# Kernel tuning notes

Measured on AMD Instinct MI355X. Metric: run time of the kernel, lower is better.

## Reference

```python
import jax, jax.numpy as jnp
import numpy as np

D_MODEL = 128
K_RED = 3          # fd_redundancy_k
MAX_ITERS = 16     # upper bound on the data-dependent while-loop; masked no-ops after convergence
NEG = -1e9


def setup_inputs() -> dict:
    key = jax.random.key(0)
    ks = jax.random.split(key, 10)
    B, U, S, D, F = 16, 2048, 512, D_MODEL, 32
    return {
        "user_enc": jax.random.normal(ks[0], (B, U, D), jnp.float32),
        "server_enc": jax.random.normal(ks[1], (B, S, D), jnp.float32),
        "users": jax.random.uniform(ks[2], (B, U, 6), jnp.float32),
        "servers": jax.random.uniform(ks[3], (B, S, 7), jnp.float32),
        "connect": jax.random.randint(ks[4], (B, U, S), 0, 2, jnp.int32),
        "fd_onehot": jax.random.randint(ks[5], (B, S, F), 0, 2, jnp.int32),
        "state_proj_w": jax.random.normal(ks[6], (D, 4), jnp.float32) * 0.05,
        "state_proj_b": jnp.zeros((D,), jnp.float32),
        "fd_bias": jnp.asarray(1.0, jnp.float32),
        "ptr_q_w": jax.random.normal(ks[7], (D, D), jnp.float32) * (D ** -0.5),
        "ptr_k_w": jax.random.normal(ks[8], (D, D), jnp.float32) * (D ** -0.5),
        "user_state_w": jax.random.normal(ks[9], (1, 3), jnp.float32) * 0.05,
        "score_bias": jnp.zeros((1,), jnp.float32),
    }


def _forward(user_enc, server_enc, users, servers, connect, fd_onehot,
             state_proj_w, state_proj_b, fd_bias, ptr_q_w, ptr_k_w,
             user_state_w, score_bias):
    B, U, _ = users.shape
    S = servers.shape[1]
    D = user_enc.shape[-1]
    needs = users[..., 2:6]                    # [B,U,4]
    init_cap = servers[..., 3:7]               # [B,S,4]
    connect_mask = connect.astype(bool)
    fd = fd_onehot.astype(jnp.float32)         # [B,S,F] in {0,1}
    F = fd.shape[-1]
    inv_sqrt_d = D ** -0.5
    tk = jnp.float32(max(K_RED, 1))
    q = user_enc @ ptr_q_w.T                   # [B,U,D]  (loop-invariant)
    u_ids = jnp.arange(U)
    s_ids = jnp.arange(S)

    def body(carry, _):
        alloc, cap, seen, logp, flag = carry
        replica_count = alloc.sum(-1)                                    # [B,U]
        need_more = replica_count < K_RED
        can_fulfill = jnp.all(cap[:, None] >= needs[:, :, None], axis=-1)  # [B,U,S]
        eligible = connect_mask & can_fulfill & need_more[..., None] & ~alloc
        go = flag & jnp.any(need_more) & jnp.any(eligible)

        # pointer-attention logits with dynamic server state
        is_new_fd = (jnp.einsum('buf,bsf->bus', seen, fd) < 0.5).astype(jnp.float32)
        cap_ratio = cap / jnp.maximum(init_cap, 1e-6)
        k_vec = (server_enc + cap_ratio @ state_proj_w.T + state_proj_b) @ ptr_k_w.T
        logits = jnp.einsum('bud,bsd->bus', q, k_vec) * inv_sqrt_d + score_bias
        logits = logits + fd_bias * is_new_fd
        rc = replica_count.astype(jnp.float32)
        user_state = jnp.stack([rc / tk,
                                jnp.clip(K_RED - rc, 0.0, None) / tk,
                                (replica_count == K_RED - 1).astype(jnp.float32)], axis=-1)
        logits = logits + user_state @ user_state_w.T                    # broadcast [B,U,1]

        cand = jnp.where(eligible, logits, NEG)
        # each valid server greedily proposes its best eligible user
        valid_server = jnp.any(eligible, axis=1)                         # [B,S]
        prop_u = jnp.argmax(cand, axis=1)                                # [B,S]
        prop_mask = valid_server[:, None, :] & (u_ids[None, :, None] == prop_u[:, None, :])
        logp_prop = jnp.max(cand, axis=1) - jax.nn.logsumexp(cand, axis=1)  # [B,S]

        # each proposed user accepts the highest-scoring proposing server
        acc_cand = jnp.where(prop_mask, logits, NEG)
        has_prop = jnp.any(prop_mask, axis=2)                            # [B,U]
        chosen_s = jnp.argmax(acc_cand, axis=2)                          # [B,U]
        accepted = has_prop[..., None] & (s_ids == chosen_s[..., None])  # [B,U,S]

        alloc = alloc | (accepted & go)
        fd_gain = (jnp.einsum('bus,bsf->buf', prop_mask.astype(jnp.float32), fd) > 0).astype(jnp.float32)
        seen = jnp.where(go, jnp.maximum(seen, fd_gain), seen)
        used = jnp.einsum('bus,buc->bsc', accepted.astype(jnp.float32), needs)
        cap = jnp.where(go, jnp.maximum(cap - used, 0.0), cap)
        gathered = jnp.take_along_axis(logp_prop, chosen_s, axis=1)      # [B,U]
        logp = logp + jnp.where(go & has_prop, gathered, 0.0)
        return (alloc, cap, seen, logp, go), None

    init = (jnp.zeros((B, U, S), bool), init_cap,
            jnp.zeros((B, U, F), jnp.float32), jnp.zeros((B, U), jnp.float32),
            jnp.asarray(True))
    (alloc, cap, seen, logp, _), _ = jax.lax.scan(body, init, None, length=MAX_ITERS)
    return logp.sum(axis=1), alloc, cap


def reference(user_enc, server_enc, users, servers, connect, fd_onehot,
              state_proj_w, state_proj_b, fd_bias, ptr_q_w, ptr_k_w,
              user_state_w, score_bias):
    # policy='greedy' branch of the original forward
    return _forward(user_enc, server_enc, users, servers, connect, fd_onehot,
                    state_proj_w, state_proj_b, fd_bias, ptr_q_w, ptr_k_w,
                    user_state_w, score_bias)
```

## Files before the change

### kernel.cpp

```cpp
#include <hip/hip_runtime.h>
#include <hip/hip_bf16.h>

#define B_N 16
#define U_N 2048
#define S_N 512
#define D_N 128
#define INV_SQRT_D 0.08838834764831845f

typedef unsigned long long ull;
typedef __attribute__((ext_vector_type(8))) short bf16x8;
typedef __attribute__((ext_vector_type(4))) float f32x4;
typedef __attribute__((ext_vector_type(4))) _Float16 f16x4;

__device__ __forceinline__ unsigned monof(float v) {
    unsigned b = __float_as_uint(v);
    return (b & 0x80000000u) ? ~b : (b | 0x80000000u);
}
__device__ __forceinline__ float unmonof(unsigned m) {
    unsigned b = (m & 0x80000000u) ? (m & 0x7fffffffu) : ~m;
    return __uint_as_float(b);
}
__device__ __forceinline__ unsigned short f2bf(float x) {
    unsigned u = __float_as_uint(x);
    return (unsigned short)((u + 0x7fffu + ((u >> 16) & 1u)) >> 16);
}

__global__ void init_state(const float* __restrict__ servers, const float* __restrict__ users,
                           const int* __restrict__ fd_onehot,
                           uint4* alloc3, unsigned* rcArr, unsigned* seenArr,
                           float* logp, float* capA, float* invA, unsigned* fdm, float* nds,
                           unsigned* frozen, float* out) {
    int i = blockIdx.x * 256 + threadIdx.x;
    if (i < B_N * U_N) {
        rcArr[i] = 0u; seenArr[i] = 0u; logp[i] = 0.f;
        alloc3[i] = make_uint4(0xFFFFFFFFu, 0xFFFFFFFFu, 0xFFFFFFFFu, 0xFFFFFFFFu);
        const float* up = users + (size_t)i * 6;
        nds[i * 4 + 0] = up[2]; nds[i * 4 + 1] = up[3];
        nds[i * 4 + 2] = up[4]; nds[i * 4 + 3] = up[5];
    }
    if (i < B_N * S_N) {
        const float* sp = servers + (size_t)i * 7;
        float4 c = make_float4(sp[3], sp[4], sp[5], sp[6]);
        ((float4*)capA)[i] = c;
        ((float4*)invA)[i] = make_float4(1.f / fmaxf(c.x, 1e-6f), 1.f / fmaxf(c.y, 1e-6f),
                                         1.f / fmaxf(c.z, 1e-6f), 1.f / fmaxf(c.w, 1e-6f));
        unsigned w = 0u;
        const int* fp = fd_onehot + (size_t)i * 32;
        #pragma unroll
        for (int f = 0; f < 32; ++f) w |= (fp[f] != 0 ? 1u : 0u) << f;
        fdm[i] = w;
    }
    if (i < 16) { frozen[i] = 0u; out[i] = 0.f; }
}

__global__ void pack_connect(const int* __restrict__ connect, ull* __restrict__ connU) {
    int i = blockIdx.x * 4 + (threadIdx.x >> 6);
    int lane = threadIdx.x & 63;
    const int* row = connect + (size_t)i * S_N;
    #pragma unroll
    for (int c = 0; c < 8; ++c) {
        ull m = __ballot(row[c * 64 + lane] != 0);
        if (lane == 0) connU[(size_t)i * 8 + c] = m;
    }
}

template <bool ABIAS, int OUTMODE>
__global__ __launch_bounds__(256) void gemm_nt(const float* __restrict__ A, const float* __restrict__ Bm,
                                               const float* __restrict__ abias, float* __restrict__ C,
                                               unsigned short* __restrict__ C16,
                                               int M, int N, int K, float scale) {
    __shared__ float As[16][68];
    __shared__ float Bs[16][68];
    int z = blockIdx.z;
    const float* Ab = A + (size_t)z * M * K;
    const float* Bb = Bm;
    int m0 = blockIdx.x * 64, n0 = blockIdx.y * 64;
    int tid = threadIdx.x;
    int tx = tid & 15, ty = tid >> 4;
    int lrow = tid >> 2, lk = (tid & 3) * 4;
    float acc[4][4] = {};
    for (int k0 = 0; k0 < K; k0 += 16) {
        float4 av = *(const float4*)(Ab + (size_t)(m0 + lrow) * K + k0 + lk);
        float4 bv = *(const float4*)(Bb + (size_t)(n0 + lrow) * K + k0 + lk);
        if (ABIAS) {
            av.x += abias[k0 + lk]; av.y += abias[k0 + lk + 1];
            av.z += abias[k0 + lk + 2]; av.w += abias[k0 + lk + 3];
        }
        __syncthreads();
        As[lk + 0][lrow] = av.x; As[lk + 1][lrow] = av.y; As[lk + 2][lrow] = av.z; As[lk + 3][lrow] = av.w;
        Bs[lk + 0][lrow] = bv.x; Bs[lk + 1][lrow] = bv.y; Bs[lk + 2][lrow] = bv.z; Bs[lk + 3][lrow] = bv.w;
        __syncthreads();
        #pragma unroll
        for (int kk = 0; kk < 16; ++kk) {
            float4 a = *(const float4*)&As[kk][ty * 4];
            float4 bq = *(const float4*)&Bs[kk][tx * 4];
            float ar[4] = {a.x, a.y, a.z, a.w}, br[4] = {bq.x, bq.y, bq.z, bq.w};
            #pragma unroll
            for (int ii = 0; ii < 4; ++ii)
                #pragma unroll
                for (int jj = 0; jj < 4; ++jj) acc[ii][jj] += ar[ii] * br[jj];
        }
    }
    #pragma unroll
    for (int ii = 0; ii < 4; ++ii) {
        float4 o = make_float4(acc[ii][0] * scale, acc[ii][1] * scale,
                               acc[ii][2] * scale, acc[ii][3] * scale);
        size_t idx = (size_t)z * M * N + (size_t)(m0 + ty * 4 + ii) * N + n0 + tx * 4;
        if (OUTMODE != 1) *(float4*)(C + idx) = o;
        if (OUTMODE != 0) {
            ushort4 ob;
            ob.x = f2bf(o.x); ob.y = f2bf(o.y); ob.z = f2bf(o.z); ob.w = f2bf(o.w);
            *(ushort4*)(C16 + idx) = ob;
        }
    }
}

__global__ void m3_kernel(const float* __restrict__ kw, const float* __restrict__ spw,
                          const float* __restrict__ qw, float* __restrict__ M3) {
    __shared__ float M2s[512];
    int t = threadIdx.x;
    {
        int d = t >> 2, c = t & 3;
        float acc = 0.f;
        for (int e = 0; e < 128; ++e) acc += kw[d * 128 + e] * spw[e * 4 + c];
        M2s[d * 4 + c] = acc * INV_SQRT_D;
    }
    __syncthreads();
    {
        int e = t >> 2, c = t & 3;
        float acc = 0.f;
        for (int d = 0; d < 128; ++d) acc += qw[d * 128 + e] * M2s[d * 4 + c];
        M3[e * 4 + c] = acc;
    }
}

__global__ void qm_kernel(const float* __restrict__ enc, const float* __restrict__ M3, float* __restrict__ qm) {
    __shared__ float qs[64][129];
    __shared__ float m3s[512];
    int b = blockIdx.y, u0 = blockIdx.x * 64;
    int t = threadIdx.x;
    for (int i = t; i < 512; i += 256) m3s[i] = M3[i];
    #pragma unroll
    for (int it = 0; it < 8; ++it) {
        int f4 = t + 256 * it;
        int row = f4 >> 5;
        int col = (f4 & 31) * 4;
        float4 v = *(const float4*)(enc + ((size_t)(b * U_N + u0 + row)) * D_N + col);
        qs[row][col] = v.x; qs[row][col + 1] = v.y; qs[row][col + 2] = v.z; qs[row][col + 3] = v.w;
    }
    __syncthreads();
    int ul = t >> 2, c = t & 3;
    float acc = 0.f;
    for (int d = 0; d < 128; ++d) acc += qs[ul][d] * m3s[d * 4 + c];
    qm[((size_t)(b * U_N + u0 + ul)) * 4 + c] = acc;
}

__global__ __launch_bounds__(256) void qk_mfma(const unsigned short* __restrict__ qb,
                                               const unsigned short* __restrict__ kb,
                                               _Float16* __restrict__ qkh) {
    const int b = blockIdx.z, u0 = blockIdx.x * 128, s0 = blockIdx.y * 64;
    const int t = threadIdx.x, w = t >> 6, l = t & 63;
    const int lr = l & 15, lq = l >> 4;
    const unsigned short* Ab = qb + ((size_t)(b * U_N + u0 + w * 32 + lr)) * D_N + lq * 8;
    const unsigned short* Bb = kb + ((size_t)(b * S_N + s0 + lr)) * D_N + lq * 8;
    f32x4 acc[2][4] = {};
    #pragma unroll
    for (int kt = 0; kt < 4; ++kt) {
        bf16x8 a0 = *(const bf16x8*)(Ab + kt * 32);
        bf16x8 a1 = *(const bf16x8*)(Ab + 16 * D_N + kt * 32);
        #pragma unroll
        for (int c = 0; c < 4; ++c) {
            bf16x8 bf = *(const bf16x8*)(Bb + c * 16 * D_N + kt * 32);
            acc[0][c] = __builtin_amdgcn_mfma_f32_16x16x32_bf16(a0, bf, acc[0][c], 0, 0, 0);
            acc[1][c] = __builtin_amdgcn_mfma_f32_16x16x32_bf16(a1, bf, acc[1][c], 0, 0, 0);
        }
    }
    __shared__ _Float16 Cs[128][72];
    #pragma unroll
    for (int mt = 0; mt < 2; ++mt)
        #pragma unroll
        for (int c = 0; c < 4; ++c)
            #pragma unroll
            for (int r = 0; r < 4; ++r)
                Cs[w * 32 + mt * 16 + lq * 4 + r][c * 16 + lr] = (_Float16)acc[mt][c][r];
    __syncthreads();
    #pragma unroll
    for (int k = 0; k < 4; ++k) {
        int row = (t >> 3) + k * 32;
        int sg = (t & 7) * 8;
        uint4 v = *(const uint4*)&Cs[row][sg];
        *(uint4*)(qkh + ((size_t)(b * U_N + u0 + row)) * S_N + s0 + sg) = v;
    }
}

__global__ __launch_bounds__(1024) void iter_fused(
    const _Float16* __restrict__ qkh, const float* __restrict__ qm4,
    const float* __restrict__ nds, const unsigned* __restrict__ connU32,
    const unsigned* __restrict__ fdm_, float* __restrict__ capA,
    const float* __restrict__ invA, const float* __restrict__ usw,
    const float* __restrict__ sbp, const float* __restrict__ fdbp,
    uint4* __restrict__ alloc3, unsigned* __restrict__ rcArr,
    unsigned* __restrict__ seenArr, float* __restrict__ logp,
    ull* __restrict__ keyP, float* __restrict__ sumP,
    unsigned* __restrict__ frozen, int iter) {
    const int bid = blockIdx.x;
    const int b = ((bid & 7) << 1) | ((bid >> 3) & 1);
    const int ublk = bid >> 4;
    if (frozen[b] != 0u) return;

    __shared__ __align__(16) char smem[56840];
    ull (*mk)[128][4] = (ull (*)[128][4])smem;
    float (*me)[128][4] = (float (*)[128][4])(smem + 32768);
    ull* ukeyL = (ull*)smem;
    unsigned* sgL = (unsigned*)(smem + 16384);
    ull* bkL = (ull*)(smem + 24576);
    float* bsL = (float*)(smem + 28672);
    float* lpL = (float*)(smem + 30720);
    float4* qmL = (float4*)(smem + 49152);
    float4* ndL = (float4*)(smem + 51200);
    uint4* alL = (uint4*)(smem + 53248);
    unsigned* rcL = (unsigned*)(smem + 55296);
    unsigned* seenL = (unsigned*)(smem + 55808);
    float* lpUL = (float*)(smem + 56320);
    unsigned* anyL = (unsigned*)(smem + 56832);

    const int tid = threadIdx.x;
    const int u0 = ublk << 7;
    const int h = tid >> 7;
    const int sl = tid & 127;
    const int s0 = sl * 4;
    const float w0 = usw[0], w1 = usw[1], w2 = usw[2], sb = sbp[0], fdb = fdbp[0];
    const float ub0 = sb + w1;
    const float ub1 = sb + w0 * (1.f / 3.f) + w1 * (2.f / 3.f);
    const float ub2 = sb + w0 * (2.f / 3.f) + w1 * (1.f / 3.f) + w2;
    const int bsb = b * S_N + s0;
    const int gub = b * U_N + u0 + h * 16;

    const _Float16* qkbase = qkh + (size_t)gub * S_N + s0;
    f16x4 qv[16];
    #pragma unroll
    for (int uu = 0; uu < 16; ++uu) qv[uu] = *(const f16x4*)(qkbase + (size_t)uu * S_N);
    float4 cap[4], iv[4]; unsigned fq[4];
    #pragma unroll
    for (int j = 0; j < 4; ++j) {
        cap[j] = ((const float4*)capA)[bsb + j];
        iv[j] = ((const float4*)invA)[bsb + j];
        fq[j] = fdm_[bsb + j];
    }
    const int cwbase = gub * 16 + (sl >> 3);
    const int nsh = (sl & 7) * 4;
    ull connbits = 0ULL;
    #pragma unroll
    for (int uu = 0; uu < 16; ++uu)
        connbits |= (ull)((connU32[cwbase + uu * 16] >> nsh) & 0xFu) << (4 * uu);
    if (tid < 128) {
        const int gu = b * U_N + u0 + tid;
        qmL[tid] = ((const float4*)qm4)[gu];
        ndL[tid] = ((const float4*)nds)[gu];
        alL[tid] = alloc3[gu];
        rcL[tid] = rcArr[gu];
        seenL[tid] = seenArr[gu];
        lpUL[tid] = logp[gu];
    }
    __syncthreads();

    if (iter > 0) {
        ukeyL[tid] = 0ULL; ukeyL[tid + 1024] = 0ULL;
        sgL[tid] = 0u; sgL[tid + 1024] = 0u;
        if (tid == 0) *anyL = 0u;
        __syncthreads();
        const int s = tid & 511, hh = tid >> 9;
        const size_t pbase = (size_t)((iter - 1) & 1) * (16 * B_N * S_N) + (size_t)b * S_N + s;
        ull best = 0ULL; float ssum = 0.f;
        #pragma unroll
        for (int j = hh * 8; j < hh * 8 + 8; ++j) {
            const ull kk = keyP[pbase + (size_t)j * (B_N * S_N)];
            best = kk > best ? kk : best;
            ssum += sumP[pbase + (size_t)j * (B_N * S_N)];
        }
        if (hh == 0) { bkL[s] = best; bsL[s] = ssum; }
        __syncthreads();
        if (hh == 1) {
            const ull ob = bkL[s];
            best = ob > best ? ob : best;
            ssum += bsL[s];
            bkL[s] = best;
            if (best != 0ULL) {
                const float mx = unmonof((unsigned)(best >> 32));
                const unsigned pu = ~(unsigned)best;
                lpL[s] = mx - __logf(ssum);
                const ull pk = ((ull)monof(mx) << 32) | (~(unsigned)s);
                atomicMax(&ukeyL[pu], pk);
                atomicOr(&sgL[pu], fdm_[b * S_N + s]);
                *anyL = 1u;
            }
        }
        __syncthreads();
        if (*anyL == 0u) {
            if (tid == 0) frozen[b] = 1u;
            return;
        }
        #pragma unroll
        for (int g = 0; g < 2; ++g) {
            const int u = tid + g * 1024;
            if ((u >> 7) == ublk) {
                const ull key = ukeyL[u];
                if (key != 0ULL) {
                    const int idx = u & 127;
                    const unsigned s2 = ~(unsigned)key;
                    uint4 al = alL[idx];
                    const unsigned r = rcL[idx];
                    if (r == 0u) al.x = s2; else if (r == 1u) al.y = s2; else al.z = s2;
                    alL[idx] = al;
                    rcL[idx] = r + 1u;
                    seenL[idx] |= sgL[u];
                    lpUL[idx] += lpL[s2];
                }
            }
        }
        #pragma unroll
        for (int j = 0; j < 4; ++j) {
            const int sj = s0 + j;
            const ull bb = bkL[sj];
            if (bb != 0ULL) {
                const unsigned pu = ~(unsigned)bb;
                if ((~(unsigned)ukeyL[pu]) == (unsigned)sj) {
                    const float4 nd = ((const float4*)nds)[b * U_N + pu];
                    cap[j].x = fmaxf(cap[j].x - nd.x, 0.f);
                    cap[j].y = fmaxf(cap[j].y - nd.y, 0.f);
                    cap[j].z = fmaxf(cap[j].z - nd.z, 0.f);
                    cap[j].w = fmaxf(cap[j].w - nd.w, 0.f);
                }
            }
        }
        __syncthreads();
        if (tid < 128) {
            const int gu = b * U_N + u0 + tid;
            alloc3[gu] = alL[tid];
            rcArr[gu] = rcL[tid];
            seenArr[gu] = seenL[tid];
            logp[gu] = lpUL[tid];
        }
        if (ublk == 0 && h == 0) {
            #pragma unroll
            for (int j = 0; j < 4; ++j) ((float4*)capA)[bsb + j] = cap[j];
        }
    }

    float4 cr[4];
    #pragma unroll
    for (int j = 0; j < 4; ++j)
        cr[j] = make_float4(cap[j].x * iv[j].x, cap[j].y * iv[j].y,
                            cap[j].z * iv[j].z, cap[j].w * iv[j].w);
    ull k[4] = {0ULL, 0ULL, 0ULL, 0ULL};
    float e[4] = {0.f, 0.f, 0.f, 0.f};
    #pragma unroll
    for (int uu = 0; uu < 16; ++uu) {
        const int idx = h * 16 + uu;
        const unsigned rcu = rcL[idx];
        if (rcu < 3u) {
            const float4 qmv = qmL[idx];
            const float4 ndv = ndL[idx];
            const unsigned snu = seenL[idx];
            const uint4 al = alL[idx];
            const unsigned nib = (unsigned)(connbits >> (4 * uu)) & 0xFu;
            const float add = (rcu == 0u) ? ub0 : ((rcu == 1u) ? ub1 : ub2);
            const unsigned uinv = ~(unsigned)(u0 + h * 16 + uu);
            #pragma unroll
            for (int j = 0; j < 4; ++j) {
                const unsigned us = (unsigned)(s0 + j);
                const bool ful = (cap[j].x >= ndv.x) & (cap[j].y >= ndv.y) &
                                 (cap[j].z >= ndv.z) & (cap[j].w >= ndv.w);
                const bool aok = (al.x != us) & (al.y != us) & (al.z != us);
                const bool el = (((nib >> j) & 1u) != 0u) & ful & aok;
                const float lg = (float)qv[uu][j] + qmv.x * cr[j].x + qmv.y * cr[j].y +
                                 qmv.z * cr[j].z + qmv.w * cr[j].w + add +
                                 (((snu & fq[j]) == 0u) ? fdb : 0.f);
                if (el) {
                    const ull kk = ((ull)monof(lg) << 32) | uinv;
                    k[j] = k[j] > kk ? k[j] : kk;
                    e[j] += __expf(lg);
                }
            }
        }
    }
    #pragma unroll
    for (int j = 0; j < 4; ++j) { mk[h][sl][j] = k[j]; me[h][sl][j] = e[j]; }
    __syncthreads();
    if (tid < 512) {
        const int sl2 = tid >> 2, j2 = tid & 3;
        ull kb2 = mk[0][sl2][j2];
        float eb = me[0][sl2][j2];
        #pragma unroll
        for (int o = 1; o < 8; ++o) {
            const ull kk = mk[o][sl2][j2];
            kb2 = kk > kb2 ? kk : kb2;
            eb += me[o][sl2][j2];
        }
        const size_t p = (size_t)(iter & 1) * (16 * B_N * S_N) +
                         (size_t)ublk * (B_N * S_N) + (size_t)b * S_N + tid;
        keyP[p] = kb2;
        sumP[p] = eb;
    }
}

__global__ __launch_bounds__(1024) void final_apply(
    const float* __restrict__ nds, const unsigned* __restrict__ fdm_,
    const float* __restrict__ capA, const uint4* __restrict__ alloc3,
    const unsigned* __restrict__ rcArr, const float* __restrict__ logp,
    const ull* __restrict__ keyP, const float* __restrict__ sumP,
    const unsigned* __restrict__ frozen, float* __restrict__ out) {
    const int bid = blockIdx.x;
    const int b = ((bid & 7) << 1) | ((bid >> 3) & 1);
    const int ublk = bid >> 4;
    __shared__ __align__(16) char smem[40324];
    ull* ukeyL = (ull*)smem;
    ull* bkL = (ull*)(smem + 16384);
    float* bsL = (float*)(smem + 20480);
    float* lpL = (float*)(smem + 22528);
    uint4* alL = (uint4*)(smem + 24576);
    unsigned* rcL = (unsigned*)(smem + 26624);
    float* lpUL = (float*)(smem + 27136);
    const int tid = threadIdx.x;
    const int u0 = ublk << 7;
    const int h = tid >> 7;
    const int sl = tid & 127;
    const int s0 = sl * 4;
    const int bsb = b * S_N + s0;
    const bool fz = (frozen[b] != 0u);

    if (tid < 128) {
        const int gu = b * U_N + u0 + tid;
        alL[tid] = alloc3[gu];
        rcL[tid] = rcArr[gu];
        lpUL[tid] = logp[gu];
    }
    float4 cap[4];
    #pragma unroll
    for (int j = 0; j < 4; ++j) cap[j] = ((const float4*)capA)[bsb + j];
    __syncthreads();

    if (!fz) {
        ukeyL[tid] = 0ULL; ukeyL[tid + 1024] = 0ULL;
        __syncthreads();
        const int s = tid & 511, hh = tid >> 9;
        const size_t pbase = (size_t)1 * (16 * B_N * S_N) + (size_t)b * S_N + s;
        ull best = 0ULL; float ssum = 0.f;
        #pragma unroll
        for (int j = hh * 8; j < hh * 8 + 8; ++j) {
            const ull kk = keyP[pbase + (size_t)j * (B_N * S_N)];
            best = kk > best ? kk : best;
            ssum += sumP[pbase + (size_t)j * (B_N * S_N)];
        }
        if (hh == 0) { bkL[s] = best; bsL[s] = ssum; }
        __syncthreads();
        if (hh == 1) {
            const ull ob = bkL[s];
            best = ob > best ? ob : best;
            ssum += bsL[s];
            bkL[s] = best;
            if (best != 0ULL) {
                const float mx = unmonof((unsigned)(best >> 32));
                const unsigned pu = ~(unsigned)best;
                lpL[s] = mx - __logf(ssum);
                const ull pk = ((ull)monof(mx) << 32) | (~(unsigned)s);
                atomicMax(&ukeyL[pu], pk);
            }
        }
        __syncthreads();
        #pragma unroll
        for (int g = 0; g < 2; ++g) {
            const int u = tid + g * 1024;
            if ((u >> 7) == ublk) {
                const ull key = ukeyL[u];
                if (key != 0ULL) {
                    const int idx = u & 127;
                    const unsigned s2 = ~(unsigned)key;
                    uint4 al = alL[idx];
                    const unsigned r = rcL[idx];
                    if (r == 0u) al.x = s2; else if (r == 1u) al.y = s2; else al.z = s2;
                    alL[idx] = al;
                    lpUL[idx] += lpL[s2];
                }
            }
        }
        #pragma unroll
        for (int j = 0; j < 4; ++j) {
            const int sj = s0 + j;
            const ull bb = bkL[sj];
            if (bb != 0ULL) {
                const unsigned pu = ~(unsigned)bb;
                if ((~(unsigned)ukeyL[pu]) == (unsigned)sj) {
                    const float4 nd = ((const float4*)nds)[b * U_N + pu];
                    cap[j].x = fmaxf(cap[j].x - nd.x, 0.f);
                    cap[j].y = fmaxf(cap[j].y - nd.y, 0.f);
                    cap[j].z = fmaxf(cap[j].z - nd.z, 0.f);
                    cap[j].w = fmaxf(cap[j].w - nd.w, 0.f);
                }
            }
        }
        __syncthreads();
    }
    const size_t orow = 16 + (size_t)(b * U_N + u0) * S_N;
    for (int i2 = tid; i2 < 128 * 128; i2 += 1024) {
        const int row = i2 >> 7;
        const unsigned c4 = (unsigned)((i2 & 127) * 4);
        const uint4 al = alL[row];
        float4 o;
        o.x = (al.x == c4 + 0u || al.y == c4 + 0u || al.z == c4 + 0u) ? 1.f : 0.f;
        o.y = (al.x == c4 + 1u || al.y == c4 + 1u || al.z == c4 + 1u) ? 1.f : 0.f;
        o.z = (al.x == c4 + 2u || al.y == c4 + 2u || al.z == c4 + 2u) ? 1.f : 0.f;
        o.w = (al.x == c4 + 3u || al.y == c4 + 3u || al.z == c4 + 3u) ? 1.f : 0.f;
        *(float4*)(out + orow + (size_t)row * S_N + c4) = o;
    }
    float sacc = (tid < 128) ? lpUL[tid] : 0.f;
    #pragma unroll
    for (int m = 1; m < 64; m <<= 1) sacc += __shfl_xor(sacc, m, 64);
    __syncthreads();
    if ((tid & 63) == 0) bsL[tid >> 6] = sacc;
    __syncthreads();
    if (tid == 0) {
        float tt = 0.f;
        #pragma unroll
        for (int i2 = 0; i2 < 16; ++i2) tt += bsL[i2];
        atomicAdd(&out[b], tt);
    }
    if (ublk == 0 && h == 0) {
        float* cdst = out + 16 + (size_t)B_N * U_N * S_N + (size_t)b * S_N * 4 + (size_t)s0 * 4;
        *(float4*)(cdst + 0) = cap[0];
        *(float4*)(cdst + 4) = cap[1];
        *(float4*)(cdst + 8) = cap[2];
        *(float4*)(cdst + 12) = cap[3];
    }
}

extern "C" void kernel_launch(void* const* d_in, const int* in_sizes, int n_in,
                              void* d_out, int out_size, void* d_ws, size_t ws_size,
                              hipStream_t stream) {
    const float* user_enc = (const float*)d_in[0];
    const float* server_enc = (const float*)d_in[1];
    const float* users = (const float*)d_in[2];
    const float* servers = (const float*)d_in[3];
    const int* connect = (const int*)d_in[4];
    const int* fd_onehot = (const int*)d_in[5];
    const float* state_proj_w = (const float*)d_in[6];
    const float* state_proj_b = (const float*)d_in[7];
    const float* fd_bias = (const float*)d_in[8];
    const float* ptr_q_w = (const float*)d_in[9];
    const float* ptr_k_w = (const float*)d_in[10];
    const float* user_state_w = (const float*)d_in[11];
    const float* score_bias = (const float*)d_in[12];
    float* out = (float*)d_out;

    char* w = (char*)d_ws;
    _Float16* qkh = (_Float16*)(w + 0);
    unsigned short* qb = (unsigned short*)(w + 33554432);
    unsigned short* kb = (unsigned short*)(w + 41943040);
    float* qm = (float*)(w + 44040192);
    ull* connU = (ull*)(w + 44564480);
    float* nds = (float*)(w + 46661632);
    unsigned* fdm = (unsigned*)(w + 47185920);
    float* capA = (float*)(w + 47218688);
    float* invA = (float*)(w + 47349760);
    float* M3 = (float*)(w + 47480832);
    unsigned* frozen = (unsigned*)(w + 47482880);
    uint4* alloc3 = (uint4*)(w + 47483136);
    unsigned* rcArr = (unsigned*)(w + 48007424);
    unsigned* seenArr = (unsigned*)(w + 48138496);
    float* logp = (float*)(w + 48269568);
    ull* keyP = (ull*)(w + 48400640);
    float* sumP = (float*)(w + 50497792);

    init_state<<<128, 256, 0, stream>>>(servers, users, fd_onehot, alloc3, rcArr, seenArr,
                                        logp, capA, invA, fdm, nds, frozen, out);
    pack_connect<<<8192, 256, 0, stream>>>(connect, connU);
    gemm_nt<true, 1><<<dim3(8, 2, 16), 256, 0, stream>>>(server_enc, ptr_k_w, state_proj_b,
                                                         nullptr, kb, S_N, D_N, D_N, INV_SQRT_D);
    gemm_nt<false, 1><<<dim3(32, 2, 16), 256, 0, stream>>>(user_enc, ptr_q_w, nullptr,
                                                           nullptr, qb, U_N, D_N, D_N, 1.0f);
    m3_kernel<<<1, 512, 0, stream>>>(ptr_k_w, state_proj_w, ptr_q_w, M3);
    qm_kernel<<<dim3(32, 16), 256, 0, stream>>>(user_enc, M3, qm);
    qk_mfma<<<dim3(16, 8, 16), 256, 0, stream>>>(qb, kb, qkh);

    for (int it = 0; it < 16; ++it)
        iter_fused<<<256, 1024, 0, stream>>>(qkh, qm, nds, (const unsigned*)connU, fdm,
                                             capA, invA, user_state_w, score_bias, fd_bias,
                                             alloc3, rcArr, seenArr, logp, keyP, sumP,
                                             frozen, it);
    final_apply<<<256, 1024, 0, stream>>>(nds, fdm, capA, alloc3, rcArr, logp,
                                          keyP, sumP, frozen, out);
}
```

Before: 417.7 us.

## Replace per-iteration kernel launches with persistent cooperative kernel using per-batch barriers

The 16 iteration launches plus the final apply kernel are merged into one cooperative persistent kernel. Per-user allocation state stays in shared memory across iterations, and the 16 blocks of each batch synchronise through a global atomic counter barrier. The M3 precompute moves into init_state so one more launch is dropped. This removes launch overhead and the global round-trips of state between iterations. In exchange it depends on cooperative launch co-residency (with a fallback path) and on spin-wait barrier latency.

```diff
diff --git a/kernel.cpp b/kernel.cpp
--- a/kernel.cpp
+++ b/kernel.cpp
@@ -29,7 +29,10 @@
                            const int* __restrict__ fd_onehot,
                            uint4* alloc3, unsigned* rcArr, unsigned* seenArr,
                            float* logp, float* capA, float* invA, unsigned* fdm, float* nds,
-                           unsigned* frozen, float* out) {
+                           unsigned* frozen, unsigned* bar, float* out,
+                           const float* __restrict__ kw, const float* __restrict__ spw,
+                           const float* __restrict__ qw, float* __restrict__ M3) {
+    __shared__ float M2s[512];
     int i = blockIdx.x * 256 + threadIdx.x;
     if (i < B_N * U_N) {
         rcArr[i] = 0u; seenArr[i] = 0u; logp[i] = 0.f;
@@ -51,6 +54,22 @@
         fdm[i] = w;
     }
     if (i < 16) { frozen[i] = 0u; out[i] = 0.f; }
+    if (i < 256) bar[i] = 0u;
+    if (blockIdx.x == 127) {
+        for (int t = threadIdx.x; t < 512; t += 256) {
+            int d = t >> 2, c = t & 3;
+            float acc = 0.f;
+            for (int e = 0; e < 128; ++e) acc += kw[d * 128 + e] * spw[e * 4 + c];
+            M2s[t] = acc * INV_SQRT_D;
+        }
+        __syncthreads();
+        for (int t = threadIdx.x; t < 512; t += 256) {
+            int e = t >> 2, c = t & 3;
+            float acc = 0.f;
+            for (int d = 0; d < 128; ++d) acc += qw[d * 128 + e] * M2s[d * 4 + c];
+            M3[t] = acc;
+        }
+    }
 }
 
 __global__ void pack_connect(const int* __restrict__ connect, ull* __restrict__ connU) {
@@ -115,25 +134,6 @@
     }
 }
 
-__global__ void m3_kernel(const float* __restrict__ kw, const float* __restrict__ spw,
-                          const float* __restrict__ qw, float* __restrict__ M3) {
-    __shared__ float M2s[512];
-    int t = threadIdx.x;
-    {
-        int d = t >> 2, c = t & 3;
-        float acc = 0.f;
-        for (int e = 0; e < 128; ++e) acc += kw[d * 128 + e] * spw[e * 4 + c];
-        M2s[d * 4 + c] = acc * INV_SQRT_D;
-    }
-    __syncthreads();
-    {
-        int e = t >> 2, c = t & 3;
-        float acc = 0.f;
-        for (int d = 0; d < 128; ++d) acc += qw[d * 128 + e] * M2s[d * 4 + c];
-        M3[e * 4 + c] = acc;
-    }
-}
-
 __global__ void qm_kernel(const float* __restrict__ enc, const float* __restrict__ M3, float* __restrict__ qm) {
     __shared__ float qs[64][129];
     __shared__ float m3s[512];
@@ -193,21 +193,14 @@
     }
 }
 
-__global__ __launch_bounds__(1024) void iter_fused(
+__global__ __launch_bounds__(1024) void alloc_loop3(
     const _Float16* __restrict__ qkh, const float* __restrict__ qm4,
     const float* __restrict__ nds, const unsigned* __restrict__ connU32,
-    const unsigned* __restrict__ fdm_, float* __restrict__ capA,
+    const unsigned* __restrict__ fdm_, const float* __restrict__ capA,
     const float* __restrict__ invA, const float* __restrict__ usw,
     const float* __restrict__ sbp, const float* __restrict__ fdbp,
-    uint4* __restrict__ alloc3, unsigned* __restrict__ rcArr,
-    unsigned* __restrict__ seenArr, float* __restrict__ logp,
     ull* __restrict__ keyP, float* __restrict__ sumP,
-    unsigned* __restrict__ frozen, int iter) {
-    const int bid = blockIdx.x;
-    const int b = ((bid & 7) << 1) | ((bid >> 3) & 1);
-    const int ublk = bid >> 4;
-    if (frozen[b] != 0u) return;
-
+    unsigned* __restrict__ bar, float* __restrict__ out) {
     __shared__ __align__(16) char smem[56840];
     ull (*mk)[128][4] = (ull (*)[128][4])smem;
     float (*me)[128][4] = (float (*)[128][4])(smem + 32768);
@@ -224,6 +217,9 @@
     float* lpUL = (float*)(smem + 56320);
     unsigned* anyL = (unsigned*)(smem + 56832);
 
+    const int bid = blockIdx.x;
+    const int b = ((bid & 7) << 1) | ((bid >> 3) & 1);
+    const int ublk = bid >> 4;
     const int tid = threadIdx.x;
     const int u0 = ublk << 7;
     const int h = tid >> 7;
@@ -257,26 +253,93 @@
         const int gu = b * U_N + u0 + tid;
         qmL[tid] = ((const float4*)qm4)[gu];
         ndL[tid] = ((const float4*)nds)[gu];
-        alL[tid] = alloc3[gu];
-        rcL[tid] = rcArr[gu];
-        seenL[tid] = seenArr[gu];
-        lpUL[tid] = logp[gu];
-    }
-    __syncthreads();
-
-    if (iter > 0) {
+        alL[tid] = make_uint4(0xFFFFFFFFu, 0xFFFFFFFFu, 0xFFFFFFFFu, 0xFFFFFFFFu);
+        rcL[tid] = 0u; seenL[tid] = 0u; lpUL[tid] = 0.f;
+    }
+    __syncthreads();
+
+    unsigned target = 0;
+    for (int iter = 0; iter < 16; ++iter) {
+        float4 cr[4];
+        #pragma unroll
+        for (int j = 0; j < 4; ++j)
+            cr[j] = make_float4(cap[j].x * iv[j].x, cap[j].y * iv[j].y,
+                                cap[j].z * iv[j].z, cap[j].w * iv[j].w);
+        ull k[4] = {0ULL, 0ULL, 0ULL, 0ULL};
+        float e[4] = {0.f, 0.f, 0.f, 0.f};
+        #pragma unroll
+        for (int uu = 0; uu < 16; ++uu) {
+            const int idx = h * 16 + uu;
+            const unsigned rcu = rcL[idx];
+            if (rcu < 3u) {
+                const float4 qmv = qmL[idx];
+                const float4 ndv = ndL[idx];
+                const unsigned snu = seenL[idx];
+                const uint4 al = alL[idx];
+                const unsigned nib = (unsigned)(connbits >> (4 * uu)) & 0xFu;
+                const float add = (rcu == 0u) ? ub0 : ((rcu == 1u) ? ub1 : ub2);
+                const unsigned uinv = ~(unsigned)(u0 + h * 16 + uu);
+                #pragma unroll
+                for (int j = 0; j < 4; ++j) {
+                    const unsigned us = (unsigned)(s0 + j);
+                    const bool ful = (cap[j].x >= ndv.x) & (cap[j].y >= ndv.y) &
+                                     (cap[j].z >= ndv.z) & (cap[j].w >= ndv.w);
+                    const bool aok = (al.x != us) & (al.y != us) & (al.z != us);
+                    const bool el = (((nib >> j) & 1u) != 0u) & ful & aok;
+                    const float lg = (float)qv[uu][j] + qmv.x * cr[j].x + qmv.y * cr[j].y +
+                                     qmv.z * cr[j].z + qmv.w * cr[j].w + add +
+                                     (((snu & fq[j]) == 0u) ? fdb : 0.f);
+                    if (el) {
+                        const ull kk = ((ull)monof(lg) << 32) | uinv;
+                        k[j] = k[j] > kk ? k[j] : kk;
+                        e[j] += __expf(lg);
+                    }
+                }
+            }
+        }
+        #pragma unroll
+        for (int j = 0; j < 4; ++j) { mk[h][sl][j] = k[j]; me[h][sl][j] = e[j]; }
+        __syncthreads();
+        if (tid < 512) {
+            const int sl2 = tid >> 2, j2 = tid & 3;
+            ull kb2 = mk[0][sl2][j2];
+            float eb = me[0][sl2][j2];
+            #pragma unroll
+            for (int o = 1; o < 8; ++o) {
+                const ull kk = mk[o][sl2][j2];
+                kb2 = kk > kb2 ? kk : kb2;
+                eb += me[o][sl2][j2];
+            }
+            const size_t p = (size_t)(iter & 1) * (16 * B_N * S_N) +
+                             (size_t)ublk * (B_N * S_N) + (size_t)b * S_N + tid;
+            __hip_atomic_store(&keyP[p], kb2, __ATOMIC_RELAXED, __HIP_MEMORY_SCOPE_AGENT);
+            __hip_atomic_store(&sumP[p], eb, __ATOMIC_RELAXED, __HIP_MEMORY_SCOPE_AGENT);
+        }
+        asm volatile("s_waitcnt vmcnt(0)" ::: "memory");
+        __syncthreads();
+        target += 16;
+        if (tid == 0) {
+            __hip_atomic_fetch_add(&bar[b * 16], 1u, __ATOMIC_RELAXED,
+                                   __HIP_MEMORY_SCOPE_AGENT);
+            while (__hip_atomic_load(&bar[b * 16], __ATOMIC_RELAXED,
+                                     __HIP_MEMORY_SCOPE_AGENT) < target)
+                __builtin_amdgcn_s_sleep(2);
+        }
+        __syncthreads();
         ukeyL[tid] = 0ULL; ukeyL[tid + 1024] = 0ULL;
         sgL[tid] = 0u; sgL[tid + 1024] = 0u;
         if (tid == 0) *anyL = 0u;
         __syncthreads();
         const int s = tid & 511, hh = tid >> 9;
-        const size_t pbase = (size_t)((iter - 1) & 1) * (16 * B_N * S_N) + (size_t)b * S_N + s;
+        const size_t pbase = (size_t)(iter & 1) * (16 * B_N * S_N) + (size_t)b * S_N + s;
         ull best = 0ULL; float ssum = 0.f;
         #pragma unroll
         for (int j = hh * 8; j < hh * 8 + 8; ++j) {
-            const ull kk = keyP[pbase + (size_t)j * (B_N * S_N)];
+            const ull kk = __hip_atomic_load(&keyP[pbase + (size_t)j * (B_N * S_N)],
+                                             __ATOMIC_RELAXED, __HIP_MEMORY_SCOPE_AGENT);
             best = kk > best ? kk : best;
-            ssum += sumP[pbase + (size_t)j * (B_N * S_N)];
+            ssum += __hip_atomic_load(&sumP[pbase + (size_t)j * (B_N * S_N)],
+                                      __ATOMIC_RELAXED, __HIP_MEMORY_SCOPE_AGENT);
         }
         if (hh == 0) { bkL[s] = best; bsL[s] = ssum; }
         __syncthreads();
@@ -296,10 +359,7 @@
             }
         }
         __syncthreads();
-        if (*anyL == 0u) {
-            if (tid == 0) frozen[b] = 1u;
-            return;
-        }
+        if (*anyL == 0u) break;
         #pragma unroll
         for (int g = 0; g < 2; ++g) {
             const int u = tid + g * 1024;
@@ -334,6 +394,177 @@
             }
         }
         __syncthreads();
+    }
+    const size_t orow = 16 + (size_t)(b * U_N + u0) * S_N;
+    for (int i2 = tid; i2 < 128 * 128; i2 += 1024) {
+        const int row = i2 >> 7;
+        const unsigned c4 = (unsigned)((i2 & 127) * 4);
+        const uint4 al = alL[row];
+        float4 o;
+        o.x = (al.x == c4 + 0u || al.y == c4 + 0u || al.z == c4 + 0u) ? 1.f : 0.f;
+        o.y = (al.x == c4 + 1u || al.y == c4 + 1u || al.z == c4 + 1u) ? 1.f : 0.f;
+        o.z = (al.x == c4 + 2u || al.y == c4 + 2u || al.z == c4 + 2u) ? 1.f : 0.f;
+        o.w = (al.x == c4 + 3u || al.y == c4 + 3u || al.z == c4 + 3u) ? 1.f : 0.f;
+        *(float4*)(out + orow + (size_t)row * S_N + c4) = o;
+    }
+    float sacc = (tid < 128) ? lpUL[tid] : 0.f;
+    #pragma unroll
+    for (int m = 1; m < 64; m <<= 1) sacc += __shfl_xor(sacc, m, 64);
+    __syncthreads();
+    if ((tid & 63) == 0) bsL[tid >> 6] = sacc;
+    __syncthreads();
+    if (tid == 0) {
+        float tt = 0.f;
+        #pragma unroll
+        for (int i2 = 0; i2 < 16; ++i2) tt += bsL[i2];
+        atomicAdd(&out[b], tt);
+    }
+    if (ublk == 0 && h == 0) {
+        float* cdst = out + 16 + (size_t)B_N * U_N * S_N + (size_t)b * S_N * 4 + (size_t)s0 * 4;
+        *(float4*)(cdst + 0) = cap[0];
+        *(float4*)(cdst + 4) = cap[1];
+        *(float4*)(cdst + 8) = cap[2];
+        *(float4*)(cdst + 12) = cap[3];
+    }
+}
+
+__global__ __launch_bounds__(1024) void iter_fused(
+    const _Float16* __restrict__ qkh, const float* __restrict__ qm4,
+    const float* __restrict__ nds, const unsigned* __restrict__ connU32,
+    const unsigned* __restrict__ fdm_, float* __restrict__ capA,
+    const float* __restrict__ invA, const float* __restrict__ usw,
+    const float* __restrict__ sbp, const float* __restrict__ fdbp,
+    uint4* __restrict__ alloc3, unsigned* __restrict__ rcArr,
+    unsigned* __restrict__ seenArr, float* __restrict__ logp,
+    ull* __restrict__ keyP, float* __restrict__ sumP,
+    unsigned* __restrict__ frozen, int iter) {
+    const int bid = blockIdx.x;
+    const int b = ((bid & 7) << 1) | ((bid >> 3) & 1);
+    const int ublk = bid >> 4;
+    if (frozen[b] != 0u) return;
+    __shared__ __align__(16) char smem[56840];
+    ull (*mk)[128][4] = (ull (*)[128][4])smem;
+    float (*me)[128][4] = (float (*)[128][4])(smem + 32768);
+    ull* ukeyL = (ull*)smem;
+    unsigned* sgL = (unsigned*)(smem + 16384);
+    ull* bkL = (ull*)(smem + 24576);
+    float* bsL = (float*)(smem + 28672);
+    float* lpL = (float*)(smem + 30720);
+    float4* qmL = (float4*)(smem + 49152);
+    float4* ndL = (float4*)(smem + 51200);
+    uint4* alL = (uint4*)(smem + 53248);
+    unsigned* rcL = (unsigned*)(smem + 55296);
+    unsigned* seenL = (unsigned*)(smem + 55808);
+    float* lpUL = (float*)(smem + 56320);
+    unsigned* anyL = (unsigned*)(smem + 56832);
+    const int tid = threadIdx.x;
+    const int u0 = ublk << 7;
+    const int h = tid >> 7;
+    const int sl = tid & 127;
+    const int s0 = sl * 4;
+    const float w0 = usw[0], w1 = usw[1], w2 = usw[2], sb = sbp[0], fdb = fdbp[0];
+    const float ub0 = sb + w1;
+    const float ub1 = sb + w0 * (1.f / 3.f) + w1 * (2.f / 3.f);
+    const float ub2 = sb + w0 * (2.f / 3.f) + w1 * (1.f / 3.f) + w2;
+    const int bsb = b * S_N + s0;
+    const int gub = b * U_N + u0 + h * 16;
+    const _Float16* qkbase = qkh + (size_t)gub * S_N + s0;
+    f16x4 qv[16];
+    #pragma unroll
+    for (int uu = 0; uu < 16; ++uu) qv[uu] = *(const f16x4*)(qkbase + (size_t)uu * S_N);
+    float4 cap[4], iv[4]; unsigned fq[4];
+    #pragma unroll
+    for (int j = 0; j < 4; ++j) {
+        cap[j] = ((const float4*)capA)[bsb + j];
+        iv[j] = ((const float4*)invA)[bsb + j];
+        fq[j] = fdm_[bsb + j];
+    }
+    const int cwbase = gub * 16 + (sl >> 3);
+    const int nsh = (sl & 7) * 4;
+    ull connbits = 0ULL;
+    #pragma unroll
+    for (int uu = 0; uu < 16; ++uu)
+        connbits |= (ull)((connU32[cwbase + uu * 16] >> nsh) & 0xFu) << (4 * uu);
+    if (tid < 128) {
+        const int gu = b * U_N + u0 + tid;
+        qmL[tid] = ((const float4*)qm4)[gu];
+        ndL[tid] = ((const float4*)nds)[gu];
+        alL[tid] = alloc3[gu];
+        rcL[tid] = rcArr[gu];
+        seenL[tid] = seenArr[gu];
+        lpUL[tid] = logp[gu];
+    }
+    __syncthreads();
+    if (iter > 0) {
+        ukeyL[tid] = 0ULL; ukeyL[tid + 1024] = 0ULL;
+        sgL[tid] = 0u; sgL[tid + 1024] = 0u;
+        if (tid == 0) *anyL = 0u;
+        __syncthreads();
+        const int s = tid & 511, hh = tid >> 9;
+        const size_t pbase = (size_t)((iter - 1) & 1) * (16 * B_N * S_N) + (size_t)b * S_N + s;
+        ull best = 0ULL; float ssum = 0.f;
+        #pragma unroll
+        for (int j = hh * 8; j < hh * 8 + 8; ++j) {
+            const ull kk = keyP[pbase + (size_t)j * (B_N * S_N)];
+            best = kk > best ? kk : best;
+            ssum += sumP[pbase + (size_t)j * (B_N * S_N)];
+        }
+        if (hh == 0) { bkL[s] = best; bsL[s] = ssum; }
+        __syncthreads();
+        if (hh == 1) {
+            const ull ob = bkL[s];
+            best = ob > best ? ob : best;
+            ssum += bsL[s];
+            bkL[s] = best;
+            if (best != 0ULL) {
+                const float mx = unmonof((unsigned)(best >> 32));
+                const unsigned pu = ~(unsigned)best;
+                lpL[s] = mx - __logf(ssum);
+                const ull pk = ((ull)monof(mx) << 32) | (~(unsigned)s);
+                atomicMax(&ukeyL[pu], pk);
+                atomicOr(&sgL[pu], fdm_[b * S_N + s]);
+                *anyL = 1u;
+            }
+        }
+        __syncthreads();
+        if (*anyL == 0u) {
+            if (tid == 0) frozen[b] = 1u;
+            return;
+        }
+        #pragma unroll
+        for (int g = 0; g < 2; ++g) {
+            const int u = tid + g * 1024;
+            if ((u >> 7) == ublk) {
+                const ull key = ukeyL[u];
+                if (key != 0ULL) {
+                    const int idx = u & 127;
+                    const unsigned s2 = ~(unsigned)key;
+                    uint4 al = alL[idx];
+                    const unsigned r = rcL[idx];
+                    if (r == 0u) al.x = s2; else if (r == 1u) al.y = s2; else al.z = s2;
+                    alL[idx] = al;
+                    rcL[idx] = r + 1u;
+                    seenL[idx] |= sgL[u];
+                    lpUL[idx] += lpL[s2];
+                }
+            }
+        }
+        #pragma unroll
+        for (int j = 0; j < 4; ++j) {
+            const int sj = s0 + j;
+            const ull bb = bkL[sj];
+            if (bb != 0ULL) {
+                const unsigned pu = ~(unsigned)bb;
+                if ((~(unsigned)ukeyL[pu]) == (unsigned)sj) {
+                    const float4 nd = ((const float4*)nds)[b * U_N + pu];
+                    cap[j].x = fmaxf(cap[j].x - nd.x, 0.f);
+                    cap[j].y = fmaxf(cap[j].y - nd.y, 0.f);
+                    cap[j].z = fmaxf(cap[j].z - nd.z, 0.f);
+                    cap[j].w = fmaxf(cap[j].w - nd.w, 0.f);
+                }
+            }
+        }
+        __syncthreads();
         if (tid < 128) {
             const int gu = b * U_N + u0 + tid;
             alloc3[gu] = alL[tid];
@@ -346,7 +577,6 @@
             for (int j = 0; j < 4; ++j) ((float4*)capA)[bsb + j] = cap[j];
         }
     }
-
     float4 cr[4];
     #pragma unroll
     for (int j = 0; j < 4; ++j)
@@ -428,7 +658,6 @@
     const int s0 = sl * 4;
     const int bsb = b * S_N + s0;
     const bool fz = (frozen[b] != 0u);
-
     if (tid < 128) {
         const int gu = b * U_N + u0 + tid;
         alL[tid] = alloc3[gu];
@@ -439,7 +668,6 @@
     #pragma unroll
     for (int j = 0; j < 4; ++j) cap[j] = ((const float4*)capA)[bsb + j];
     __syncthreads();
-
     if (!fz) {
         ukeyL[tid] = 0ULL; ukeyL[tid + 1024] = 0ULL;
         __syncthreads();
@@ -564,29 +792,41 @@
     float* invA = (float*)(w + 47349760);
     float* M3 = (float*)(w + 47480832);
     unsigned* frozen = (unsigned*)(w + 47482880);
-    uint4* alloc3 = (uint4*)(w + 47483136);
-    unsigned* rcArr = (unsigned*)(w + 48007424);
-    unsigned* seenArr = (unsigned*)(w + 48138496);
-    float* logp = (float*)(w + 48269568);
-    ull* keyP = (ull*)(w + 48400640);
-    float* sumP = (float*)(w + 50497792);
+    unsigned* bar = (unsigned*)(w + 47483136);
+    uint4* alloc3 = (uint4*)(w + 47484160);
+    unsigned* rcArr = (unsigned*)(w + 48008448);
+    unsigned* seenArr = (unsigned*)(w + 48139520);
+    float* logp = (float*)(w + 48270592);
+    ull* keyP = (ull*)(w + 48401664);
+    float* sumP = (float*)(w + 50498816);
 
     init_state<<<128, 256, 0, stream>>>(servers, users, fd_onehot, alloc3, rcArr, seenArr,
-                                        logp, capA, invA, fdm, nds, frozen, out);
+                                        logp, capA, invA, fdm, nds, frozen, bar, out,
+                                        ptr_k_w, state_proj_w, ptr_q_w, M3);
     pack_connect<<<8192, 256, 0, stream>>>(connect, connU);
     gemm_nt<true, 1><<<dim3(8, 2, 16), 256, 0, stream>>>(server_enc, ptr_k_w, state_proj_b,
                                                          nullptr, kb, S_N, D_N, D_N, INV_SQRT_D);
     gemm_nt<false, 1><<<dim3(32, 2, 16), 256, 0, stream>>>(user_enc, ptr_q_w, nullptr,
                                                            nullptr, qb, U_N, D_N, D_N, 1.0f);
-    m3_kernel<<<1, 512, 0, stream>>>(ptr_k_w, state_proj_w, ptr_q_w, M3);
     qm_kernel<<<dim3(32, 16), 256, 0, stream>>>(user_enc, M3, qm);
     qk_mfma<<<dim3(16, 8, 16), 256, 0, stream>>>(qb, kb, qkh);
 
-    for (int it = 0; it < 16; ++it)
-        iter_fused<<<256, 1024, 0, stream>>>(qkh, qm, nds, (const unsigned*)connU, fdm,
-                                             capA, invA, user_state_w, score_bias, fd_bias,
-                                             alloc3, rcArr, seenArr, logp, keyP, sumP,
-                                             frozen, it);
-    final_apply<<<256, 1024, 0, stream>>>(nds, fdm, capA, alloc3, rcArr, logp,
-                                          keyP, sumP, frozen, out);
-}
+    const unsigned* connU32c = (const unsigned*)connU;
+    const unsigned* fdmc = (const unsigned*)fdm;
+    void* args[] = {(void*)&qkh, (void*)&qm, (void*)&nds, (void*)&connU32c,
+                    (void*)&fdmc, (void*)&capA, (void*)&invA,
+                    (void*)&user_state_w, (void*)&score_bias, (void*)&fd_bias,
+                    (void*)&keyP, (void*)&sumP, (void*)&bar, (void*)&out};
+    hipError_t cerr = hipLaunchCooperativeKernel((const void*)alloc_loop3, dim3(256), dim3(1024),
+                                                 args, 0, stream);
+    if (cerr != hipSuccess) {
+        (void)hipGetLastError();
+        for (int it = 0; it < 16; ++it)
+            iter_fused<<<256, 1024, 0, stream>>>(qkh, qm, nds, (const unsigned*)connU, fdm,
+                                                 capA, invA, user_state_w, score_bias, fd_bias,
+                                                 alloc3, rcArr, seenArr, logp, keyP, sumP,
+                                                 frozen, it);
+        final_apply<<<256, 1024, 0, stream>>>(nds, fdm, capA, alloc3, rcArr, logp,
+                                              keyP, sumP, frozen, out);
+    }
+}
```

Result: slower. 586.9 us (+40.5%).

## Merge setup kernels and skip qk loads for saturated users in iteration

Applied to the files above, without the earlier changes.

Six preprocessing kernels become two. One kernel packs connect, initialises state and computes M3, and a second runs both projection GEMMs plus the qm projection in a single grid. This cuts launch count and serialisation between small kernels. Inside the per-iteration kernel, the fp16 qk tile loads now happen only for users whose replica count is still below three, which cuts redundant global reads in later iterations. The loads move after the shared-memory sync, which may reduce overlap of load latency with setup.

```diff
diff --git a/kernel.cpp b/kernel.cpp
--- a/kernel.cpp
+++ b/kernel.cpp
@@ -25,64 +25,114 @@
     return (unsigned short)((u + 0x7fffu + ((u >> 16) & 1u)) >> 16);
 }
 
-__global__ void init_state(const float* __restrict__ servers, const float* __restrict__ users,
-                           const int* __restrict__ fd_onehot,
-                           uint4* alloc3, unsigned* rcArr, unsigned* seenArr,
-                           float* logp, float* capA, float* invA, unsigned* fdm, float* nds,
-                           unsigned* frozen, float* out) {
-    int i = blockIdx.x * 256 + threadIdx.x;
-    if (i < B_N * U_N) {
+__global__ __launch_bounds__(256) void prep(
+    const int* __restrict__ connect, ull* __restrict__ connU,
+    const float* __restrict__ servers, const float* __restrict__ users,
+    const int* __restrict__ fd_onehot,
+    uint4* alloc3, unsigned* rcArr, unsigned* seenArr,
+    float* logp, float* capA, float* invA, unsigned* fdm, float* nds,
+    unsigned* frozen, float* out,
+    const float* __restrict__ kw, const float* __restrict__ spw,
+    const float* __restrict__ qw, float* __restrict__ M3) {
+    __shared__ float M2s[512];
+    const int tid = threadIdx.x;
+    {
+        const int i4 = blockIdx.x * 4 + (tid >> 6);
+        const int lane = tid & 63;
+        const int* row = connect + (size_t)i4 * S_N;
+        #pragma unroll
+        for (int c = 0; c < 8; ++c) {
+            ull m = __ballot(row[c * 64 + lane] != 0);
+            if (lane == 0) connU[(size_t)i4 * 8 + c] = m;
+        }
+    }
+    if (blockIdx.x < 128) {
+        const int i = blockIdx.x * 256 + tid;
         rcArr[i] = 0u; seenArr[i] = 0u; logp[i] = 0.f;
         alloc3[i] = make_uint4(0xFFFFFFFFu, 0xFFFFFFFFu, 0xFFFFFFFFu, 0xFFFFFFFFu);
         const float* up = users + (size_t)i * 6;
         nds[i * 4 + 0] = up[2]; nds[i * 4 + 1] = up[3];
         nds[i * 4 + 2] = up[4]; nds[i * 4 + 3] = up[5];
-    }
-    if (i < B_N * S_N) {
-        const float* sp = servers + (size_t)i * 7;
-        float4 c = make_float4(sp[3], sp[4], sp[5], sp[6]);
-        ((float4*)capA)[i] = c;
-        ((float4*)invA)[i] = make_float4(1.f / fmaxf(c.x, 1e-6f), 1.f / fmaxf(c.y, 1e-6f),
-                                         1.f / fmaxf(c.z, 1e-6f), 1.f / fmaxf(c.w, 1e-6f));
-        unsigned w = 0u;
-        const int* fp = fd_onehot + (size_t)i * 32;
-        #pragma unroll
-        for (int f = 0; f < 32; ++f) w |= (fp[f] != 0 ? 1u : 0u) << f;
-        fdm[i] = w;
-    }
-    if (i < 16) { frozen[i] = 0u; out[i] = 0.f; }
-}
-
-__global__ void pack_connect(const int* __restrict__ connect, ull* __restrict__ connU) {
-    int i = blockIdx.x * 4 + (threadIdx.x >> 6);
-    int lane = threadIdx.x & 63;
-    const int* row = connect + (size_t)i * S_N;
-    #pragma unroll
-    for (int c = 0; c < 8; ++c) {
-        ull m = __ballot(row[c * 64 + lane] != 0);
-        if (lane == 0) connU[(size_t)i * 8 + c] = m;
-    }
-}
-
-template <bool ABIAS, int OUTMODE>
-__global__ __launch_bounds__(256) void gemm_nt(const float* __restrict__ A, const float* __restrict__ Bm,
-                                               const float* __restrict__ abias, float* __restrict__ C,
-                                               unsigned short* __restrict__ C16,
-                                               int M, int N, int K, float scale) {
-    __shared__ float As[16][68];
-    __shared__ float Bs[16][68];
-    int z = blockIdx.z;
-    const float* Ab = A + (size_t)z * M * K;
-    const float* Bb = Bm;
-    int m0 = blockIdx.x * 64, n0 = blockIdx.y * 64;
-    int tid = threadIdx.x;
-    int tx = tid & 15, ty = tid >> 4;
-    int lrow = tid >> 2, lk = (tid & 3) * 4;
+        if (i < B_N * S_N) {
+            const float* sp = servers + (size_t)i * 7;
+            float4 c = make_float4(sp[3], sp[4], sp[5], sp[6]);
+            ((float4*)capA)[i] = c;
+            ((float4*)invA)[i] = make_float4(1.f / fmaxf(c.x, 1e-6f), 1.f / fmaxf(c.y, 1e-6f),
+                                             1.f / fmaxf(c.z, 1e-6f), 1.f / fmaxf(c.w, 1e-6f));
+            unsigned w = 0u;
+            const int* fp = fd_onehot + (size_t)i * 32;
+            #pragma unroll
+            for (int f = 0; f < 32; ++f) w |= (fp[f] != 0 ? 1u : 0u) << f;
+            fdm[i] = w;
+        }
+        if (i < 16) { frozen[i] = 0u; out[i] = 0.f; }
+    }
+    if (blockIdx.x == 127) {
+        for (int t = tid; t < 512; t += 256) {
+            int d = t >> 2, c = t & 3;
+            float acc = 0.f;
+            for (int e = 0; e < 128; ++e) acc += kw[d * 128 + e] * spw[e * 4 + c];
+            M2s[t] = acc * INV_SQRT_D;
+        }
+        __syncthreads();
+        for (int t = tid; t < 512; t += 256) {
+            int e = t >> 2, c = t & 3;
+            float acc = 0.f;
+            for (int d = 0; d < 128; ++d) acc += qw[d * 128 + e] * M2s[d * 4 + c];
+            M3[t] = acc;
+        }
+    }
+}
+
+__global__ __launch_bounds__(256) void gemm2(
+    const float* __restrict__ user_enc, const float* __restrict__ server_enc,
+    const float* __restrict__ qw, const float* __restrict__ kw,
+    const float* __restrict__ spb, const float* __restrict__ M3,
+    unsigned short* __restrict__ qb, unsigned short* __restrict__ kb,
+    float* __restrict__ qm) {
+    __shared__ float smemF[64 * 129 + 512];
+    const int x = blockIdx.x, y = blockIdx.y, z = blockIdx.z;
+    const int tid = threadIdx.x;
+    if (x >= 40) {
+        if (y != 0) return;
+        float (*qs)[129] = (float (*)[129])smemF;
+        float* m3s = smemF + 64 * 129;
+        const int b = z, u0 = (x - 40) * 64;
+        for (int i = tid; i < 512; i += 256) m3s[i] = M3[i];
+        #pragma unroll
+        for (int it = 0; it < 8; ++it) {
+            int f4 = tid + 256 * it;
+            int rowi = f4 >> 5;
+            int col = (f4 & 31) * 4;
+            float4 v = *(const float4*)(user_enc + ((size_t)(b * U_N + u0 + rowi)) * D_N + col);
+            qs[rowi][col] = v.x; qs[rowi][col + 1] = v.y;
+            qs[rowi][col + 2] = v.z; qs[rowi][col + 3] = v.w;
+        }
+        __syncthreads();
+        const int ul = tid >> 2, c = tid & 3;
+        float acc = 0.f;
+        for (int d = 0; d < 128; ++d) acc += qs[ul][d] * m3s[d * 4 + c];
+        qm[((size_t)(b * U_N + u0 + ul)) * 4 + c] = acc;
+        return;
+    }
+    const bool isK = (x < 8);
+    const float* A = isK ? server_enc : user_enc;
+    const float* Bm = isK ? kw : qw;
+    const float* abias = isK ? spb : nullptr;
+    unsigned short* C16 = isK ? kb : qb;
+    const int M = isK ? S_N : U_N;
+    const float scale = isK ? INV_SQRT_D : 1.0f;
+    const int m0 = (isK ? x : (x - 8)) * 64, n0 = y * 64;
+    float (*As)[68] = (float (*)[68])smemF;
+    float (*Bs)[68] = (float (*)[68])(smemF + 16 * 68);
+    const float* Ab = A + (size_t)z * M * D_N;
+    const int tx = tid & 15, ty = tid >> 4;
+    const int lrow = tid >> 2, lk = (tid & 3) * 4;
     float acc[4][4] = {};
-    for (int k0 = 0; k0 < K; k0 += 16) {
-        float4 av = *(const float4*)(Ab + (size_t)(m0 + lrow) * K + k0 + lk);
-        float4 bv = *(const float4*)(Bb + (size_t)(n0 + lrow) * K + k0 + lk);
-        if (ABIAS) {
+    for (int k0 = 0; k0 < D_N; k0 += 16) {
+        float4 av = *(const float4*)(Ab + (size_t)(m0 + lrow) * D_N + k0 + lk);
+        float4 bv = *(const float4*)(Bm + (size_t)(n0 + lrow) * D_N + k0 + lk);
+        if (abias) {
             av.x += abias[k0 + lk]; av.y += abias[k0 + lk + 1];
             av.z += abias[k0 + lk + 2]; av.w += abias[k0 + lk + 3];
         }
@@ -103,56 +153,12 @@
     }
     #pragma unroll
     for (int ii = 0; ii < 4; ++ii) {
-        float4 o = make_float4(acc[ii][0] * scale, acc[ii][1] * scale,
-                               acc[ii][2] * scale, acc[ii][3] * scale);
-        size_t idx = (size_t)z * M * N + (size_t)(m0 + ty * 4 + ii) * N + n0 + tx * 4;
-        if (OUTMODE != 1) *(float4*)(C + idx) = o;
-        if (OUTMODE != 0) {
-            ushort4 ob;
-            ob.x = f2bf(o.x); ob.y = f2bf(o.y); ob.z = f2bf(o.z); ob.w = f2bf(o.w);
-            *(ushort4*)(C16 + idx) = ob;
-        }
-    }
-}
-
-__global__ void m3_kernel(const float* __restrict__ kw, const float* __restrict__ spw,
-                          const float* __restrict__ qw, float* __restrict__ M3) {
-    __shared__ float M2s[512];
-    int t = threadIdx.x;
-    {
-        int d = t >> 2, c = t & 3;
-        float acc = 0.f;
-        for (int e = 0; e < 128; ++e) acc += kw[d * 128 + e] * spw[e * 4 + c];
-        M2s[d * 4 + c] = acc * INV_SQRT_D;
-    }
-    __syncthreads();
-    {
-        int e = t >> 2, c = t & 3;
-        float acc = 0.f;
-        for (int d = 0; d < 128; ++d) acc += qw[d * 128 + e] * M2s[d * 4 + c];
-        M3[e * 4 + c] = acc;
-    }
-}
-
-__global__ void qm_kernel(const float* __restrict__ enc, const float* __restrict__ M3, float* __restrict__ qm) {
-    __shared__ float qs[64][129];
-    __shared__ float m3s[512];
-    int b = blockIdx.y, u0 = blockIdx.x * 64;
-    int t = threadIdx.x;
-    for (int i = t; i < 512; i += 256) m3s[i] = M3[i];
-    #pragma unroll
-    for (int it = 0; it < 8; ++it) {
-        int f4 = t + 256 * it;
-        int row = f4 >> 5;
-        int col = (f4 & 31) * 4;
-        float4 v = *(const float4*)(enc + ((size_t)(b * U_N + u0 + row)) * D_N + col);
-        qs[row][col] = v.x; qs[row][col + 1] = v.y; qs[row][col + 2] = v.z; qs[row][col + 3] = v.w;
-    }
-    __syncthreads();
-    int ul = t >> 2, c = t & 3;
-    float acc = 0.f;
-    for (int d = 0; d < 128; ++d) acc += qs[ul][d] * m3s[d * 4 + c];
-    qm[((size_t)(b * U_N + u0 + ul)) * 4 + c] = acc;
+        size_t idx = (size_t)z * M * D_N + (size_t)(m0 + ty * 4 + ii) * D_N + n0 + tx * 4;
+        ushort4 ob;
+        ob.x = f2bf(acc[ii][0] * scale); ob.y = f2bf(acc[ii][1] * scale);
+        ob.z = f2bf(acc[ii][2] * scale); ob.w = f2bf(acc[ii][3] * scale);
+        *(ushort4*)(C16 + idx) = ob;
+    }
 }
 
 __global__ __launch_bounds__(256) void qk_mfma(const unsigned short* __restrict__ qb,
@@ -236,10 +242,6 @@
     const int bsb = b * S_N + s0;
     const int gub = b * U_N + u0 + h * 16;
 
-    const _Float16* qkbase = qkh + (size_t)gub * S_N + s0;
-    f16x4 qv[16];
-    #pragma unroll
-    for (int uu = 0; uu < 16; ++uu) qv[uu] = *(const f16x4*)(qkbase + (size_t)uu * S_N);
     float4 cap[4], iv[4]; unsigned fq[4];
     #pragma unroll
     for (int j = 0; j < 4; ++j) {
@@ -263,6 +265,15 @@
         lpUL[tid] = logp[gu];
     }
     __syncthreads();
+    unsigned actmask = 0u;
+    #pragma unroll
+    for (int uu = 0; uu < 16; ++uu)
+        actmask |= (rcL[h * 16 + uu] < 3u ? 1u : 0u) << uu;
+    const _Float16* qkbase = qkh + (size_t)gub * S_N + s0;
+    f16x4 qv[16] = {};
+    #pragma unroll
+    for (int uu = 0; uu < 16; ++uu)
+        if ((actmask >> uu) & 1u) qv[uu] = *(const f16x4*)(qkbase + (size_t)uu * S_N);
 
     if (iter > 0) {
         ukeyL[tid] = 0ULL; ukeyL[tid + 1024] = 0ULL;
@@ -571,15 +582,11 @@
     ull* keyP = (ull*)(w + 48400640);
     float* sumP = (float*)(w + 50497792);
 
-    init_state<<<128, 256, 0, stream>>>(servers, users, fd_onehot, alloc3, rcArr, seenArr,
-                                        logp, capA, invA, fdm, nds, frozen, out);
-    pack_connect<<<8192, 256, 0, stream>>>(connect, connU);
-    gemm_nt<true, 1><<<dim3(8, 2, 16), 256, 0, stream>>>(server_enc, ptr_k_w, state_proj_b,
-                                                         nullptr, kb, S_N, D_N, D_N, INV_SQRT_D);
-    gemm_nt<false, 1><<<dim3(32, 2, 16), 256, 0, stream>>>(user_enc, ptr_q_w, nullptr,
-                                                           nullptr, qb, U_N, D_N, D_N, 1.0f);
-    m3_kernel<<<1, 512, 0, stream>>>(ptr_k_w, state_proj_w, ptr_q_w, M3);
-    qm_kernel<<<dim3(32, 16), 256, 0, stream>>>(user_enc, M3, qm);
+    prep<<<8192, 256, 0, stream>>>(connect, connU, servers, users, fd_onehot,
+                                   alloc3, rcArr, seenArr, logp, capA, invA, fdm, nds,
+                                   frozen, out, ptr_k_w, state_proj_w, ptr_q_w, M3);
+    gemm2<<<dim3(72, 2, 16), 256, 0, stream>>>(user_enc, server_enc, ptr_q_w, ptr_k_w,
+                                               state_proj_b, M3, qb, kb, qm);
     qk_mfma<<<dim3(16, 8, 16), 256, 0, stream>>>(qb, kb, qkh);
 
     for (int it = 0; it < 16; ++it)
```

Result: no change. 418.6 us (+0.2%).
